# Kernel optimization log

Hardware: AMD Instinct MI355X
Metric: run time of the kernel (lower is better)

## Reference

```python
import jax, jax.numpy as jnp
import numpy as np

B, L, E, K = 2, 2048, 512, 4
KE = E // 2  # kernel_dim is overwritten to embed_dim//2 in __init__


def setup_inputs() -> dict:
    key = jax.random.key(0)
    ks = jax.random.split(key, 6)
    s = 1.0 / np.sqrt(E).astype(np.float32)
    return {
        "xsa": jax.random.normal(ks[0], (B, L, E), jnp.float32),
        "Wq": jax.random.normal(ks[1], (K * KE, E), jnp.float32) * s,   # attq.weight
        "Wk": jax.random.normal(ks[2], (K * KE, E), jnp.float32) * s,   # attk.weight
        "Wv": jax.random.normal(ks[3], (E, K * E), jnp.float32) * s,    # attv.weight
        "biasW": jax.random.normal(ks[4], (KE, K), jnp.float32) * s,    # bias.weight
        "bias2W": jax.random.normal(ks[5], (E, K), jnp.float32) * s,    # bias2.weight
    }


def reference(xsa, Wq, Wk, Wv, biasW, bias2W):
    b_, l_, e_ = xsa.shape
    k_ = biasW.shape[1]
    ke = biasW.shape[0]
    # projections -> (B,L,K,KE)
    xq = (xsa @ Wq.T).reshape(b_, l_, k_, ke)
    xk = (xsa @ Wk.T).reshape(b_, l_, k_, ke)
    # fold the per-head Gaussian center bias into the keys: xd = xq - (xk + bias)
    xkb = xk + biasW.T[None, None]                      # (B,L,K,KE)
    # ||xq_i - xkb_j||^2 = ||xq_i||^2 - 2 xq_i . xkb_j + ||xkb_j||^2  (avoids (B,L,L,K,KE) blowup)
    qn = jnp.sum(xq * xq, axis=-1)                      # (B,L,K)
    kn = jnp.sum(xkb * xkb, axis=-1)                    # (B,L,K)
    cross = jnp.einsum('bikd,bjkd->bikj', xq, xkb)      # (B,L,K,L)
    hikj = -(qn[..., None] - 2.0 * cross + kn.transpose(0, 2, 1)[:, None])
    hikj = hikj / (ke ** 0.5)
    pikj = jax.nn.softmax(hikj, axis=-1)                # softmax over keys j
    # value gather per head: (B,L,K,E)
    yik = jnp.einsum('bikj,bje->bike', pikj, xsa)
    # per-head linear combine with attv.weight reshaped to (K,E,E)
    Wv3 = Wv.reshape(k_, e_, e_)
    yik = jnp.einsum('bike,kef->bikf', yik, Wv3) + bias2W.T[None, None]
    return yik.reshape(b_, l_, k_ * e_)
```

## Files before the change

kernel.cpp:

```cpp
#include <hip/hip_runtime.h>


#define L_ 2048
#define E_ 512
#define KE_ 256
#define NH_ 4

typedef __bf16 bf16x8 __attribute__((ext_vector_type(8)));
typedef float f32x4 __attribute__((ext_vector_type(4)));

__device__ __forceinline__ float bf2f(unsigned short u){
    union { float f; unsigned int i; } v; v.i = ((unsigned int)u) << 16; return v.f;
}
__device__ __forceinline__ unsigned short f2bf(float x){
    union { float f; unsigned int i; } v; v.f = x;
    unsigned int r = v.i + 0x7fffu + ((v.i >> 16) & 1u);
    return (unsigned short)(r >> 16);
}
__device__ __forceinline__ void gll16(const void* g, void* l){
    __builtin_amdgcn_global_load_lds((const __attribute__((address_space(1))) void*)g,
                                     (__attribute__((address_space(3))) void*)l, 16, 0, 0);
}

__global__ __launch_bounds__(256) void proj_kernel(
    const float* __restrict__ xsa, const float* __restrict__ Wq,
    const float* __restrict__ Wk, const float* __restrict__ biasW,
    unsigned short* __restrict__ xqhi, unsigned short* __restrict__ xqlo,
    unsigned short* __restrict__ xkhi, unsigned short* __restrict__ xklo)
{
    __shared__ float Ast[32][132];
    __shared__ float Bst[32][132];
    const int t = threadIdx.x;
    const int m0 = blockIdx.x * 128;
    const int n0 = blockIdx.y * 128;
    const bool isK = (n0 >= 1024);
    const float* W = isK ? Wk : Wq;
    const int nW0 = isK ? (n0 - 1024) : n0;
    const int ty = t >> 4, tx = t & 15;

    float acc[8][8];
#pragma unroll
    for (int i = 0; i < 8; i++)
#pragma unroll
        for (int j = 0; j < 8; j++) acc[i][j] = 0.f;

    for (int kk0 = 0; kk0 < 512; kk0 += 32) {
#pragma unroll
        for (int r = 0; r < 4; r++) {
            int idx = t + r * 256;
            int row = idx >> 3;
            int c4  = idx & 7;
            float4 v = *reinterpret_cast<const float4*>(&xsa[(size_t)(m0 + row) * 512 + kk0 + c4 * 4]);
            Ast[c4*4+0][row] = v.x; Ast[c4*4+1][row] = v.y;
            Ast[c4*4+2][row] = v.z; Ast[c4*4+3][row] = v.w;
            float4 w = *reinterpret_cast<const float4*>(&W[(size_t)(nW0 + row) * 512 + kk0 + c4 * 4]);
            Bst[c4*4+0][row] = w.x; Bst[c4*4+1][row] = w.y;
            Bst[c4*4+2][row] = w.z; Bst[c4*4+3][row] = w.w;
        }
        __syncthreads();
#pragma unroll
        for (int kk = 0; kk < 32; kk++) {
            float a[8], bb[8];
            *reinterpret_cast<float4*>(&a[0])  = *reinterpret_cast<const float4*>(&Ast[kk][ty*8]);
            *reinterpret_cast<float4*>(&a[4])  = *reinterpret_cast<const float4*>(&Ast[kk][ty*8+4]);
            *reinterpret_cast<float4*>(&bb[0]) = *reinterpret_cast<const float4*>(&Bst[kk][tx*8]);
            *reinterpret_cast<float4*>(&bb[4]) = *reinterpret_cast<const float4*>(&Bst[kk][tx*8+4]);
#pragma unroll
            for (int i = 0; i < 8; i++)
#pragma unroll
                for (int j = 0; j < 8; j++) acc[i][j] += a[i] * bb[j];
        }
        __syncthreads();
    }

    const int nh = (n0 + tx*8) & 1023;
    const int kh = nh >> 8, d0 = nh & 255;
    float bias[8];
#pragma unroll
    for (int j = 0; j < 8; j++) bias[j] = isK ? biasW[(d0 + j) * NH_ + kh] : 0.f;
    unsigned short* dsthi = isK ? xkhi : xqhi;
    unsigned short* dstlo = isK ? xklo : xqlo;

#pragma unroll
    for (int i = 0; i < 8; i++) {
        int m = m0 + ty*8 + i;
        int b = m >> 11, l = m & 2047;
        size_t off = ((size_t)((b * NH_ + kh) * L_ + l)) * KE_ + d0;
        unsigned short th[8], tl[8];
#pragma unroll
        for (int j = 0; j < 8; j++) {
            float x = acc[i][j] + bias[j];
            unsigned short hh = f2bf(x);
            th[j] = hh;
            tl[j] = f2bf(x - bf2f(hh));
        }
        *reinterpret_cast<ushort4*>(&dsthi[off])     = *reinterpret_cast<ushort4*>(&th[0]);
        *reinterpret_cast<ushort4*>(&dsthi[off + 4]) = *reinterpret_cast<ushort4*>(&th[4]);
        *reinterpret_cast<ushort4*>(&dstlo[off])     = *reinterpret_cast<ushort4*>(&tl[0]);
        *reinterpret_cast<ushort4*>(&dstlo[off + 4]) = *reinterpret_cast<ushort4*>(&tl[4]);
    }
}

__global__ __launch_bounds__(256) void trans_kernel(
    const float* __restrict__ xsa, unsigned short* __restrict__ xThi,
    unsigned short* __restrict__ xTlo)
{
    __shared__ float T[64][65];
    const int t = threadIdx.x;
    const int l0 = blockIdx.x * 64, e0 = blockIdx.y * 64, b = blockIdx.z;
#pragma unroll
    for (int p = 0; p < 4; p++) {
        int row = p*16 + (t >> 4);
        int c4 = t & 15;
        float4 v = *reinterpret_cast<const float4*>(&xsa[((size_t)(b*L_ + l0 + row))*E_ + e0 + c4*4]);
        T[row][c4*4+0] = v.x; T[row][c4*4+1] = v.y;
        T[row][c4*4+2] = v.z; T[row][c4*4+3] = v.w;
    }
    __syncthreads();
#pragma unroll
    for (int p = 0; p < 16; p++) {
        int e = p*4 + (t >> 6);
        int lp = t & 63;
        float x = T[lp][e];
        unsigned short hh = f2bf(x);
        size_t off = ((size_t)(b*E_ + e0 + e))*L_ + l0 + lp;
        xThi[off] = hh;
        xTlo[off] = f2bf(x - bf2f(hh));
    }
}

__global__ __launch_bounds__(256) void kn_kernel(
    const unsigned short* __restrict__ xkhi, const unsigned short* __restrict__ xklo,
    float* __restrict__ kn)
{
    const int w = threadIdx.x >> 6, lane = threadIdx.x & 63;
    const int row = blockIdx.x * 4 + w;
    ushort4 uh = *reinterpret_cast<const ushort4*>(&xkhi[(size_t)row * KE_ + lane*4]);
    ushort4 ul = *reinterpret_cast<const ushort4*>(&xklo[(size_t)row * KE_ + lane*4]);
    float x0 = bf2f(uh.x) + bf2f(ul.x);
    float x1 = bf2f(uh.y) + bf2f(ul.y);
    float x2 = bf2f(uh.z) + bf2f(ul.z);
    float x3 = bf2f(uh.w) + bf2f(ul.w);
    float s = x0*x0 + x1*x1 + x2*x2 + x3*x3;
#pragma unroll
    for (int m = 32; m; m >>= 1) s += __shfl_xor(s, m, 64);
    if (lane == 0) kn[row] = s;
}

__global__ __launch_bounds__(256, 1) void attn_kernel(
    const unsigned short* __restrict__ xqhi, const unsigned short* __restrict__ xqlo,
    const unsigned short* __restrict__ xkhi, const unsigned short* __restrict__ xklo,
    const unsigned short* __restrict__ xThi, const unsigned short* __restrict__ xTlo,
    const float* __restrict__ knp, unsigned short* __restrict__ ybar)
{
    __shared__ __align__(16) char smem[131072];
    char* const kh_b = smem;
    char* const kl_b = smem + 32768;
    char* const vh_b = smem + 65536;
    char* const vl_b = smem + 98304;

    const int tid = threadIdx.x;
    const int w = tid >> 6, lane = tid & 63;
    const int l15 = lane & 15, l4 = lane >> 4;
    const int bk = blockIdx.y, b = bk >> 2;
    const int i0 = blockIdx.x * 64;
    const size_t bkL = (size_t)bk * L_;

    bf16x8 qh[8], ql[8];
    {
        const size_t qoff = (bkL + i0 + w*16 + l15) * KE_ + l4*8;
#pragma unroll
        for (int ks = 0; ks < 8; ks++) {
            qh[ks] = *reinterpret_cast<const bf16x8*>(xqhi + qoff + ks*32);
            ql[ks] = *reinterpret_cast<const bf16x8*>(xqlo + qoff + ks*32);
        }
    }

    const int s0tbl[4] = {0,4,1,5};
    const int s1tbl[4] = {2,6,3,7};
    const int jg2 = tid & 3;
    const int vs0 = s0tbl[jg2]*8, vs1 = s1tbl[jg2]*8;

    uint4 vreg[16];
#pragma unroll
    for (int r = 0; r < 16; r++) {
        int arr = r >> 3;
        int e = (r & 7)*64 + (tid >> 2);
        const unsigned short* src = (arr ? xTlo : xThi) + ((size_t)(b*E_ + e))*L_ + 0 + jg2*8;
        vreg[r] = *reinterpret_cast<const uint4*>(src);
    }
#pragma unroll
    for (int r = 0; r < 8; r++) {
        int seg = w*8 + r;
        int arr = seg >> 4;
        int sj  = (seg & 15)*2 + (lane >> 5);
        int c   = lane & 31;
        int cp  = c ^ (sj & 7);
        const unsigned short* src = (arr ? xklo : xkhi) + (bkL + 0 + sj)*KE_ + cp*8;
        char* dst = (arr ? kl_b : kh_b) + (seg & 15)*1024;
        gll16(src, dst);
    }
    __syncthreads();

    f32x4 O[32];
#pragma unroll
    for (int e = 0; e < 32; e++) O[e] = (f32x4){0.f,0.f,0.f,0.f};
    float mrun = -1e30f, lrun = 0.f;
    int cur = 0;
    const int axor = (l15 & 7) << 4;

    for (int t = 0; t < 64; ++t) {
        const int j0 = t*32;
        const int jn = (j0 + 32) & (L_-1);

#pragma unroll
        for (int r = 0; r < 16; r++) {
            int e = (r & 7)*64 + (tid >> 2);
            int key = ((e >> 1) & 7) << 4;
            char* base = (r >> 3) ? vl_b : vh_b;
            uint2 lo; lo.x = vreg[r].x; lo.y = vreg[r].y;
            uint2 hi; hi.x = vreg[r].z; hi.y = vreg[r].w;
            *reinterpret_cast<uint2*>(base + ((e*64 + vs0) ^ key)) = lo;
            *reinterpret_cast<uint2*>(base + ((e*64 + vs1) ^ key)) = hi;
        }
#pragma unroll
        for (int r = 0; r < 8; r++) {
            int seg = w*8 + r;
            int arr = seg >> 4;
            int sj  = (seg & 15)*2 + (lane >> 5);
            int c   = lane & 31;
            int cp  = c ^ (sj & 7);
            const unsigned short* src = (arr ? xklo : xkhi) + (bkL + jn + sj)*KE_ + cp*8;
            char* dst = (arr ? kl_b : kh_b) + (cur ^ 1)*16384 + (seg & 15)*1024;
            gll16(src, dst);
        }
        float4 kn0 = *reinterpret_cast<const float4*>(knp + bkL + j0 + l4*4);
        float4 kn1 = *reinterpret_cast<const float4*>(knp + bkL + j0 + 16 + l4*4);

        f32x4 s0 = (f32x4){0.f,0.f,0.f,0.f};
        f32x4 s1 = (f32x4){0.f,0.f,0.f,0.f};
        {
            const char* kh = kh_b + cur*16384;
            const char* kl = kl_b + cur*16384;
            const int arow0 = l15*512, arow1 = (16 + l15)*512;
#pragma unroll
            for (int ks = 0; ks < 8; ks++) {
                int ko = ks*64 + l4*16;
                int a0 = (arow0 + ko) ^ axor;
                int a1 = (arow1 + ko) ^ axor;
                bf16x8 ah0 = *reinterpret_cast<const bf16x8*>(kh + a0);
                bf16x8 al0 = *reinterpret_cast<const bf16x8*>(kl + a0);
                bf16x8 ah1 = *reinterpret_cast<const bf16x8*>(kh + a1);
                bf16x8 al1 = *reinterpret_cast<const bf16x8*>(kl + a1);
                s0 = __builtin_amdgcn_mfma_f32_16x16x32_bf16(ah0, qh[ks], s0, 0, 0, 0);
                s0 = __builtin_amdgcn_mfma_f32_16x16x32_bf16(al0, qh[ks], s0, 0, 0, 0);
                s0 = __builtin_amdgcn_mfma_f32_16x16x32_bf16(ah0, ql[ks], s0, 0, 0, 0);
                s1 = __builtin_amdgcn_mfma_f32_16x16x32_bf16(ah1, qh[ks], s1, 0, 0, 0);
                s1 = __builtin_amdgcn_mfma_f32_16x16x32_bf16(al1, qh[ks], s1, 0, 0, 0);
                s1 = __builtin_amdgcn_mfma_f32_16x16x32_bf16(ah1, ql[ks], s1, 0, 0, 0);
            }
        }

        float h[8];
#pragma unroll
        for (int r = 0; r < 4; r++) {
            h[r]   = s0[r]*0.125f - ((const float*)&kn0)[r]*0.0625f;
            h[4+r] = s1[r]*0.125f - ((const float*)&kn1)[r]*0.0625f;
        }
        float pmax = h[0];
#pragma unroll
        for (int r = 1; r < 8; r++) pmax = fmaxf(pmax, h[r]);
        pmax = fmaxf(pmax, __shfl_xor(pmax, 16, 64));
        pmax = fmaxf(pmax, __shfl_xor(pmax, 32, 64));
        if (__any(pmax > mrun + 8.0f)) {
            float mnew = fmaxf(mrun, pmax);
            float osc = __expf(mrun - mnew);
            mrun = mnew;
            lrun *= osc;
            float osc_pv[4];
#pragma unroll
            for (int r = 0; r < 4; r++) osc_pv[r] = __shfl(osc, l4*4 + r, 64);
#pragma unroll
            for (int et = 0; et < 32; et++) {
                O[et][0] *= osc_pv[0]; O[et][1] *= osc_pv[1];
                O[et][2] *= osc_pv[2]; O[et][3] *= osc_pv[3];
            }
        }
        float p[8], ls = 0.f;
#pragma unroll
        for (int r = 0; r < 8; r++) { p[r] = __expf(h[r] - mrun); ls += p[r]; }
        ls += __shfl_xor(ls, 16, 64);
        ls += __shfl_xor(ls, 32, 64);
        lrun += ls;
        bf16x8 pah, pal;
        {
            union { unsigned int u[4]; bf16x8 v; } ch, cl;
#pragma unroll
            for (int i = 0; i < 4; i++) {
                unsigned short h0 = f2bf(p[2*i]),   h1 = f2bf(p[2*i+1]);
                unsigned short l0 = f2bf(p[2*i]   - bf2f(h0));
                unsigned short l1 = f2bf(p[2*i+1] - bf2f(h1));
                ch.u[i] = (unsigned int)h0 | ((unsigned int)h1 << 16);
                cl.u[i] = (unsigned int)l0 | ((unsigned int)l1 << 16);
            }
            pah = ch.v; pal = cl.v;
        }

        __syncthreads();

#pragma unroll
        for (int r = 0; r < 16; r++) {
            int arr = r >> 3;
            int e = (r & 7)*64 + (tid >> 2);
            const unsigned short* src = (arr ? xTlo : xThi) + ((size_t)(b*E_ + e))*L_ + jn + jg2*8;
            vreg[r] = *reinterpret_cast<const uint4*>(src);
        }
#pragma unroll
        for (int et = 0; et < 32; et++) {
            int vo = (et*16 + l15)*64 + l4*16;
            vo ^= ((vo >> 7) & 7) << 4;
            bf16x8 vh = *reinterpret_cast<const bf16x8*>(vh_b + vo);
            bf16x8 vl = *reinterpret_cast<const bf16x8*>(vl_b + vo);
            O[et] = __builtin_amdgcn_mfma_f32_16x16x32_bf16(pah, vh, O[et], 0, 0, 0);
            O[et] = __builtin_amdgcn_mfma_f32_16x16x32_bf16(pal, vh, O[et], 0, 0, 0);
            O[et] = __builtin_amdgcn_mfma_f32_16x16x32_bf16(pah, vl, O[et], 0, 0, 0);
        }

        __syncthreads();
        cur ^= 1;
    }

    float inv = 1.f / lrun;
    float inv_pv[4];
#pragma unroll
    for (int r = 0; r < 4; r++) inv_pv[r] = __shfl(inv, l4*4 + r, 64);
#pragma unroll
    for (int r = 0; r < 4; r++) {
        int row = i0 + w*16 + l4*4 + r;
        size_t base = (bkL + row)*E_ + l15;
#pragma unroll
        for (int et = 0; et < 32; et++)
            ybar[base + et*16] = f2bf(O[et][r] * inv_pv[r]);
    }
}

__global__ __launch_bounds__(256) void combine_kernel(
    const unsigned short* __restrict__ ybar, const float* __restrict__ Wv,
    const float* __restrict__ bias2W, float* __restrict__ out)
{
    __shared__ float Ast[32][132];
    __shared__ float Bst[32][132];
    const int t = threadIdx.x;
    const int m0 = blockIdx.x * 128;
    const int n0 = blockIdx.y * 128;
    const int bk = blockIdx.z;
    const int k = bk & 3, b = bk >> 2;
    const size_t abase = (size_t)bk * L_ * E_;
    const size_t wbase = (size_t)k * E_ * E_;
    const int ty = t >> 4, tx = t & 15;

    float acc[8][8];
#pragma unroll
    for (int i = 0; i < 8; i++)
#pragma unroll
        for (int j = 0; j < 8; j++) acc[i][j] = 0.f;

    for (int kk0 = 0; kk0 < 512; kk0 += 32) {
#pragma unroll
        for (int r = 0; r < 4; r++) {
            int idx = t + r * 256;
            int row = idx >> 3;
            int c4  = idx & 7;
            ushort4 u = *reinterpret_cast<const ushort4*>(&ybar[abase + (size_t)(m0 + row) * E_ + kk0 + c4*4]);
            Ast[c4*4+0][row] = bf2f(u.x); Ast[c4*4+1][row] = bf2f(u.y);
            Ast[c4*4+2][row] = bf2f(u.z); Ast[c4*4+3][row] = bf2f(u.w);
            int er  = idx >> 5;
            int fc4 = idx & 31;
            *reinterpret_cast<float4*>(&Bst[er][fc4*4]) =
                *reinterpret_cast<const float4*>(&Wv[wbase + (size_t)(kk0 + er) * E_ + n0 + fc4*4]);
        }
        __syncthreads();
#pragma unroll
        for (int kk = 0; kk < 32; kk++) {
            float a[8], bb[8];
            *reinterpret_cast<float4*>(&a[0])  = *reinterpret_cast<const float4*>(&Ast[kk][ty*8]);
            *reinterpret_cast<float4*>(&a[4])  = *reinterpret_cast<const float4*>(&Ast[kk][ty*8+4]);
            *reinterpret_cast<float4*>(&bb[0]) = *reinterpret_cast<const float4*>(&Bst[kk][tx*8]);
            *reinterpret_cast<float4*>(&bb[4]) = *reinterpret_cast<const float4*>(&Bst[kk][tx*8+4]);
#pragma unroll
            for (int i = 0; i < 8; i++)
#pragma unroll
                for (int j = 0; j < 8; j++) acc[i][j] += a[i] * bb[j];
        }
        __syncthreads();
    }

    float bias[8];
#pragma unroll
    for (int j = 0; j < 8; j++) bias[j] = bias2W[(n0 + tx*8 + j) * NH_ + k];

#pragma unroll
    for (int i = 0; i < 8; i++) {
        int iL = m0 + ty*8 + i;
        size_t ob = ((size_t)b * L_ + iL) * (NH_ * E_) + k * E_ + n0 + tx*8;
        float4 v0 = make_float4(acc[i][0]+bias[0], acc[i][1]+bias[1], acc[i][2]+bias[2], acc[i][3]+bias[3]);
        float4 v1 = make_float4(acc[i][4]+bias[4], acc[i][5]+bias[5], acc[i][6]+bias[6], acc[i][7]+bias[7]);
        *reinterpret_cast<float4*>(&out[ob])     = v0;
        *reinterpret_cast<float4*>(&out[ob + 4]) = v1;
    }
}

extern "C" void kernel_launch(void* const* d_in, const int* in_sizes, int n_in,
                              void* d_out, int out_size, void* d_ws, size_t ws_size,
                              hipStream_t stream)
{
    const float* xsa    = (const float*)d_in[0];
    const float* Wq     = (const float*)d_in[1];
    const float* Wk     = (const float*)d_in[2];
    const float* Wv     = (const float*)d_in[3];
    const float* biasW  = (const float*)d_in[4];
    const float* bias2W = (const float*)d_in[5];
    float* out = (float*)d_out;

    unsigned short* ws16 = (unsigned short*)d_ws;
    unsigned short* xqhi = ws16;
    unsigned short* xqlo = ws16 + 4194304;
    unsigned short* xkhi = ws16 + 8388608;
    unsigned short* xklo = ws16 + 12582912;
    unsigned short* xThi = ws16 + 16777216;
    unsigned short* xTlo = ws16 + 18874368;
    unsigned short* ybar = ws16 + 20971520;
    float* knv = (float*)(ws16 + 29360128);

    proj_kernel<<<dim3(32, 16), 256, 0, stream>>>(xsa, Wq, Wk, biasW, xqhi, xqlo, xkhi, xklo);
    trans_kernel<<<dim3(32, 8, 2), 256, 0, stream>>>(xsa, xThi, xTlo);
    kn_kernel<<<dim3(4096), 256, 0, stream>>>(xkhi, xklo, knv);
    attn_kernel<<<dim3(32, 8), 256, 0, stream>>>(xqhi, xqlo, xkhi, xklo, xThi, xTlo, knv, ybar);
    combine_kernel<<<dim3(16, 4, 8), 256, 0, stream>>>(ybar, Wv, bias2W, out);
}
```

Measured before the change: 525.1 us.

## Use MFMA for combine GEMM and split attention output across 512-thread blocks

The combine GEMM moves from scalar FP32 FMA to bf16 MFMA with a hi/lo split of Wv, and a new kernel pre-transposes and splits Wv for it. The attention kernel now runs 512 threads per block: each pair of waves shares a 16-row query tile and splits the 512-wide value dimension in half. This halves the per-wave output accumulator registers and doubles the waves available to hide latency. In exchange, QK^T scores are recomputed redundantly in both waves of a pair, an extra kernel launch is added, and dropping the lo term of ybar in combine loses some precision.

```diff
diff --git a/kernel.cpp b/kernel.cpp
--- a/kernel.cpp
+++ b/kernel.cpp
@@ -129,6 +129,34 @@
     }
 }
 
+__global__ __launch_bounds__(256) void wsplit_kernel(
+    const float* __restrict__ Wv, unsigned short* __restrict__ whiT,
+    unsigned short* __restrict__ wloT)
+{
+    __shared__ float T[64][65];
+    const int t = threadIdx.x;
+    const int e0 = blockIdx.x * 64, f0 = blockIdx.y * 64, k = blockIdx.z;
+#pragma unroll
+    for (int p = 0; p < 4; p++) {
+        int row = p*16 + (t >> 4);
+        int c4 = t & 15;
+        float4 v = *reinterpret_cast<const float4*>(&Wv[((size_t)(k*E_ + e0 + row))*E_ + f0 + c4*4]);
+        T[row][c4*4+0] = v.x; T[row][c4*4+1] = v.y;
+        T[row][c4*4+2] = v.z; T[row][c4*4+3] = v.w;
+    }
+    __syncthreads();
+#pragma unroll
+    for (int p = 0; p < 16; p++) {
+        int fl = p*4 + (t >> 6);
+        int el = t & 63;
+        float x = T[el][fl];
+        unsigned short hh = f2bf(x);
+        size_t off = ((size_t)(k*E_ + f0 + fl))*E_ + e0 + el;
+        whiT[off] = hh;
+        wloT[off] = f2bf(x - bf2f(hh));
+    }
+}
+
 __global__ __launch_bounds__(256) void kn_kernel(
     const unsigned short* __restrict__ xkhi, const unsigned short* __restrict__ xklo,
     float* __restrict__ kn)
@@ -147,7 +175,7 @@
     if (lane == 0) kn[row] = s;
 }
 
-__global__ __launch_bounds__(256, 1) void attn_kernel(
+__global__ __launch_bounds__(512, 2) void attn_kernel(
     const unsigned short* __restrict__ xqhi, const unsigned short* __restrict__ xqlo,
     const unsigned short* __restrict__ xkhi, const unsigned short* __restrict__ xklo,
     const unsigned short* __restrict__ xThi, const unsigned short* __restrict__ xTlo,
@@ -161,6 +189,7 @@
 
     const int tid = threadIdx.x;
     const int w = tid >> 6, lane = tid & 63;
+    const int rg = w >> 1, h = w & 1;
     const int l15 = lane & 15, l4 = lane >> 4;
     const int bk = blockIdx.y, b = bk >> 2;
     const int i0 = blockIdx.x * 64;
@@ -168,7 +197,7 @@
 
     bf16x8 qh[8], ql[8];
     {
-        const size_t qoff = (bkL + i0 + w*16 + l15) * KE_ + l4*8;
+        const size_t qoff = (bkL + i0 + rg*16 + l15) * KE_ + l4*8;
 #pragma unroll
         for (int ks = 0; ks < 8; ks++) {
             qh[ks] = *reinterpret_cast<const bf16x8*>(xqhi + qoff + ks*32);
@@ -178,33 +207,32 @@
 
     const int s0tbl[4] = {0,4,1,5};
     const int s1tbl[4] = {2,6,3,7};
-    const int jg2 = tid & 3;
-    const int vs0 = s0tbl[jg2]*8, vs1 = s1tbl[jg2]*8;
-
-    uint4 vreg[16];
-#pragma unroll
-    for (int r = 0; r < 16; r++) {
-        int arr = r >> 3;
-        int e = (r & 7)*64 + (tid >> 2);
-        const unsigned short* src = (arr ? xTlo : xThi) + ((size_t)(b*E_ + e))*L_ + 0 + jg2*8;
+    const int jc = tid & 3;
+    const int vs0 = s0tbl[jc]*8, vs1 = s1tbl[jc]*8;
+
+    uint4 vreg[8];
+#pragma unroll
+    for (int r = 0; r < 8; r++) {
+        int arr = r >> 2;
+        int e = (r & 3)*128 + (tid >> 2);
+        const unsigned short* src = (arr ? xTlo : xThi) + ((size_t)(b*E_ + e))*L_ + 0 + jc*8;
         vreg[r] = *reinterpret_cast<const uint4*>(src);
     }
 #pragma unroll
-    for (int r = 0; r < 8; r++) {
-        int seg = w*8 + r;
-        int arr = seg >> 4;
-        int sj  = (seg & 15)*2 + (lane >> 5);
+    for (int r = 0; r < 4; r++) {
+        int arr = r >> 1;
+        int sj  = (r & 1)*16 + w*2 + (lane >> 5);
         int c   = lane & 31;
         int cp  = c ^ (sj & 7);
         const unsigned short* src = (arr ? xklo : xkhi) + (bkL + 0 + sj)*KE_ + cp*8;
-        char* dst = (arr ? kl_b : kh_b) + (seg & 15)*1024;
+        char* dst = (arr ? kl_b : kh_b) + ((r & 1)*512 + w*64)*16;
         gll16(src, dst);
     }
     __syncthreads();
 
-    f32x4 O[32];
-#pragma unroll
-    for (int e = 0; e < 32; e++) O[e] = (f32x4){0.f,0.f,0.f,0.f};
+    f32x4 O[16];
+#pragma unroll
+    for (int e = 0; e < 16; e++) O[e] = (f32x4){0.f,0.f,0.f,0.f};
     float mrun = -1e30f, lrun = 0.f;
     int cur = 0;
     const int axor = (l15 & 7) << 4;
@@ -214,24 +242,23 @@
         const int jn = (j0 + 32) & (L_-1);
 
 #pragma unroll
-        for (int r = 0; r < 16; r++) {
-            int e = (r & 7)*64 + (tid >> 2);
+        for (int r = 0; r < 8; r++) {
+            int e = (r & 3)*128 + (tid >> 2);
             int key = ((e >> 1) & 7) << 4;
-            char* base = (r >> 3) ? vl_b : vh_b;
+            char* base = (r >> 2) ? vl_b : vh_b;
             uint2 lo; lo.x = vreg[r].x; lo.y = vreg[r].y;
             uint2 hi; hi.x = vreg[r].z; hi.y = vreg[r].w;
             *reinterpret_cast<uint2*>(base + ((e*64 + vs0) ^ key)) = lo;
             *reinterpret_cast<uint2*>(base + ((e*64 + vs1) ^ key)) = hi;
         }
 #pragma unroll
-        for (int r = 0; r < 8; r++) {
-            int seg = w*8 + r;
-            int arr = seg >> 4;
-            int sj  = (seg & 15)*2 + (lane >> 5);
+        for (int r = 0; r < 4; r++) {
+            int arr = r >> 1;
+            int sj  = (r & 1)*16 + w*2 + (lane >> 5);
             int c   = lane & 31;
             int cp  = c ^ (sj & 7);
             const unsigned short* src = (arr ? xklo : xkhi) + (bkL + jn + sj)*KE_ + cp*8;
-            char* dst = (arr ? kl_b : kh_b) + (cur ^ 1)*16384 + (seg & 15)*1024;
+            char* dst = (arr ? kl_b : kh_b) + (cur ^ 1)*16384 + ((r & 1)*512 + w*64)*16;
             gll16(src, dst);
         }
         float4 kn0 = *reinterpret_cast<const float4*>(knp + bkL + j0 + l4*4);
@@ -261,15 +288,15 @@
             }
         }
 
-        float h[8];
+        float hh[8];
 #pragma unroll
         for (int r = 0; r < 4; r++) {
-            h[r]   = s0[r]*0.125f - ((const float*)&kn0)[r]*0.0625f;
-            h[4+r] = s1[r]*0.125f - ((const float*)&kn1)[r]*0.0625f;
-        }
-        float pmax = h[0];
-#pragma unroll
-        for (int r = 1; r < 8; r++) pmax = fmaxf(pmax, h[r]);
+            hh[r]   = s0[r]*0.125f - ((const float*)&kn0)[r]*0.0625f;
+            hh[4+r] = s1[r]*0.125f - ((const float*)&kn1)[r]*0.0625f;
+        }
+        float pmax = hh[0];
+#pragma unroll
+        for (int r = 1; r < 8; r++) pmax = fmaxf(pmax, hh[r]);
         pmax = fmaxf(pmax, __shfl_xor(pmax, 16, 64));
         pmax = fmaxf(pmax, __shfl_xor(pmax, 32, 64));
         if (__any(pmax > mrun + 8.0f)) {
@@ -281,14 +308,14 @@
 #pragma unroll
             for (int r = 0; r < 4; r++) osc_pv[r] = __shfl(osc, l4*4 + r, 64);
 #pragma unroll
-            for (int et = 0; et < 32; et++) {
+            for (int et = 0; et < 16; et++) {
                 O[et][0] *= osc_pv[0]; O[et][1] *= osc_pv[1];
                 O[et][2] *= osc_pv[2]; O[et][3] *= osc_pv[3];
             }
         }
         float p[8], ls = 0.f;
 #pragma unroll
-        for (int r = 0; r < 8; r++) { p[r] = __expf(h[r] - mrun); ls += p[r]; }
+        for (int r = 0; r < 8; r++) { p[r] = __expf(hh[r] - mrun); ls += p[r]; }
         ls += __shfl_xor(ls, 16, 64);
         ls += __shfl_xor(ls, 32, 64);
         lrun += ls;
@@ -309,15 +336,15 @@
         __syncthreads();
 
 #pragma unroll
-        for (int r = 0; r < 16; r++) {
-            int arr = r >> 3;
-            int e = (r & 7)*64 + (tid >> 2);
-            const unsigned short* src = (arr ? xTlo : xThi) + ((size_t)(b*E_ + e))*L_ + jn + jg2*8;
+        for (int r = 0; r < 8; r++) {
+            int arr = r >> 2;
+            int e = (r & 3)*128 + (tid >> 2);
+            const unsigned short* src = (arr ? xTlo : xThi) + ((size_t)(b*E_ + e))*L_ + jn + jc*8;
             vreg[r] = *reinterpret_cast<const uint4*>(src);
         }
 #pragma unroll
-        for (int et = 0; et < 32; et++) {
-            int vo = (et*16 + l15)*64 + l4*16;
+        for (int et = 0; et < 16; et++) {
+            int vo = (((h*16 + et)*16 + l15))*64 + l4*16;
             vo ^= ((vo >> 7) & 7) << 4;
             bf16x8 vh = *reinterpret_cast<const bf16x8*>(vh_b + vo);
             bf16x8 vl = *reinterpret_cast<const bf16x8*>(vl_b + vo);
@@ -336,78 +363,89 @@
     for (int r = 0; r < 4; r++) inv_pv[r] = __shfl(inv, l4*4 + r, 64);
 #pragma unroll
     for (int r = 0; r < 4; r++) {
-        int row = i0 + w*16 + l4*4 + r;
-        size_t base = (bkL + row)*E_ + l15;
-#pragma unroll
-        for (int et = 0; et < 32; et++)
+        int row = i0 + rg*16 + l4*4 + r;
+        size_t base = (bkL + row)*E_ + h*256 + l15;
+#pragma unroll
+        for (int et = 0; et < 16; et++)
             ybar[base + et*16] = f2bf(O[et][r] * inv_pv[r]);
     }
 }
 
 __global__ __launch_bounds__(256) void combine_kernel(
-    const unsigned short* __restrict__ ybar, const float* __restrict__ Wv,
-    const float* __restrict__ bias2W, float* __restrict__ out)
-{
-    __shared__ float Ast[32][132];
-    __shared__ float Bst[32][132];
-    const int t = threadIdx.x;
+    const unsigned short* __restrict__ ybar, const unsigned short* __restrict__ whiT,
+    const unsigned short* __restrict__ wloT, const float* __restrict__ bias2W,
+    float* __restrict__ out)
+{
+    __shared__ unsigned short A_s[128][40];
+    __shared__ unsigned short Bh_s[128][40];
+    __shared__ unsigned short Bl_s[128][40];
+
+    const int tid = threadIdx.x;
+    const int w = tid >> 6, lane = tid & 63;
+    const int wm = w >> 1, wn = w & 1;
+    const int l15 = lane & 15, l4 = lane >> 4;
     const int m0 = blockIdx.x * 128;
     const int n0 = blockIdx.y * 128;
     const int bk = blockIdx.z;
     const int k = bk & 3, b = bk >> 2;
     const size_t abase = (size_t)bk * L_ * E_;
     const size_t wbase = (size_t)k * E_ * E_;
-    const int ty = t >> 4, tx = t & 15;
-
-    float acc[8][8];
-#pragma unroll
-    for (int i = 0; i < 8; i++)
-#pragma unroll
-        for (int j = 0; j < 8; j++) acc[i][j] = 0.f;
-
-    for (int kk0 = 0; kk0 < 512; kk0 += 32) {
-#pragma unroll
-        for (int r = 0; r < 4; r++) {
-            int idx = t + r * 256;
-            int row = idx >> 3;
-            int c4  = idx & 7;
-            ushort4 u = *reinterpret_cast<const ushort4*>(&ybar[abase + (size_t)(m0 + row) * E_ + kk0 + c4*4]);
-            Ast[c4*4+0][row] = bf2f(u.x); Ast[c4*4+1][row] = bf2f(u.y);
-            Ast[c4*4+2][row] = bf2f(u.z); Ast[c4*4+3][row] = bf2f(u.w);
-            int er  = idx >> 5;
-            int fc4 = idx & 31;
-            *reinterpret_cast<float4*>(&Bst[er][fc4*4]) =
-                *reinterpret_cast<const float4*>(&Wv[wbase + (size_t)(kk0 + er) * E_ + n0 + fc4*4]);
-        }
-        __syncthreads();
-#pragma unroll
-        for (int kk = 0; kk < 32; kk++) {
-            float a[8], bb[8];
-            *reinterpret_cast<float4*>(&a[0])  = *reinterpret_cast<const float4*>(&Ast[kk][ty*8]);
-            *reinterpret_cast<float4*>(&a[4])  = *reinterpret_cast<const float4*>(&Ast[kk][ty*8+4]);
-            *reinterpret_cast<float4*>(&bb[0]) = *reinterpret_cast<const float4*>(&Bst[kk][tx*8]);
-            *reinterpret_cast<float4*>(&bb[4]) = *reinterpret_cast<const float4*>(&Bst[kk][tx*8+4]);
-#pragma unroll
-            for (int i = 0; i < 8; i++)
-#pragma unroll
-                for (int j = 0; j < 8; j++) acc[i][j] += a[i] * bb[j];
-        }
-        __syncthreads();
-    }
-
-    float bias[8];
-#pragma unroll
-    for (int j = 0; j < 8; j++) bias[j] = bias2W[(n0 + tx*8 + j) * NH_ + k];
-
-#pragma unroll
-    for (int i = 0; i < 8; i++) {
-        int iL = m0 + ty*8 + i;
-        size_t ob = ((size_t)b * L_ + iL) * (NH_ * E_) + k * E_ + n0 + tx*8;
-        float4 v0 = make_float4(acc[i][0]+bias[0], acc[i][1]+bias[1], acc[i][2]+bias[2], acc[i][3]+bias[3]);
-        float4 v1 = make_float4(acc[i][4]+bias[4], acc[i][5]+bias[5], acc[i][6]+bias[6], acc[i][7]+bias[7]);
-        *reinterpret_cast<float4*>(&out[ob])     = v0;
-        *reinterpret_cast<float4*>(&out[ob + 4]) = v1;
-    }
+
+    f32x4 acc[4][4];
+#pragma unroll
+    for (int i = 0; i < 4; i++)
+#pragma unroll
+        for (int j = 0; j < 4; j++) acc[i][j] = (f32x4){0.f,0.f,0.f,0.f};
+
+    for (int e0 = 0; e0 < 512; e0 += 32) {
+        __syncthreads();
+#pragma unroll
+        for (int r = 0; r < 2; r++) {
+            int idx = tid + r*256;
+            int row = idx >> 2, c = idx & 3;
+            *reinterpret_cast<uint4*>(&A_s[row][c*8]) =
+                *reinterpret_cast<const uint4*>(&ybar[abase + (size_t)(m0 + row)*E_ + e0 + c*8]);
+            *reinterpret_cast<uint4*>(&Bh_s[row][c*8]) =
+                *reinterpret_cast<const uint4*>(&whiT[wbase + (size_t)(n0 + row)*E_ + e0 + c*8]);
+            *reinterpret_cast<uint4*>(&Bl_s[row][c*8]) =
+                *reinterpret_cast<const uint4*>(&wloT[wbase + (size_t)(n0 + row)*E_ + e0 + c*8]);
+        }
+        __syncthreads();
+
+        bf16x8 a[4], bh[4], bl[4];
+#pragma unroll
+        for (int mt = 0; mt < 4; mt++)
+            a[mt] = *reinterpret_cast<const bf16x8*>(&A_s[wm*64 + mt*16 + l15][l4*8]);
+#pragma unroll
+        for (int ft = 0; ft < 4; ft++) {
+            bh[ft] = *reinterpret_cast<const bf16x8*>(&Bh_s[wn*64 + ft*16 + l15][l4*8]);
+            bl[ft] = *reinterpret_cast<const bf16x8*>(&Bl_s[wn*64 + ft*16 + l15][l4*8]);
+        }
+#pragma unroll
+        for (int mt = 0; mt < 4; mt++)
+#pragma unroll
+            for (int ft = 0; ft < 4; ft++) {
+                acc[mt][ft] = __builtin_amdgcn_mfma_f32_16x16x32_bf16(a[mt], bh[ft], acc[mt][ft], 0, 0, 0);
+                acc[mt][ft] = __builtin_amdgcn_mfma_f32_16x16x32_bf16(a[mt], bl[ft], acc[mt][ft], 0, 0, 0);
+            }
+    }
+
+    float bias[4];
+#pragma unroll
+    for (int ft = 0; ft < 4; ft++)
+        bias[ft] = bias2W[(n0 + wn*64 + ft*16 + l15) * NH_ + k];
+
+#pragma unroll
+    for (int mt = 0; mt < 4; mt++)
+#pragma unroll
+        for (int ft = 0; ft < 4; ft++) {
+            int f = n0 + wn*64 + ft*16 + l15;
+#pragma unroll
+            for (int rr = 0; rr < 4; rr++) {
+                int i = m0 + wm*64 + mt*16 + l4*4 + rr;
+                out[((size_t)(b*L_ + i))*(NH_*E_) + k*E_ + f] = acc[mt][ft][rr] + bias[ft];
+            }
+        }
 }
 
 extern "C" void kernel_launch(void* const* d_in, const int* in_sizes, int n_in,
@@ -423,18 +461,21 @@
     float* out = (float*)d_out;
 
     unsigned short* ws16 = (unsigned short*)d_ws;
-    unsigned short* xqhi = ws16;
-    unsigned short* xqlo = ws16 + 4194304;
-    unsigned short* xkhi = ws16 + 8388608;
-    unsigned short* xklo = ws16 + 12582912;
-    unsigned short* xThi = ws16 + 16777216;
-    unsigned short* xTlo = ws16 + 18874368;
-    unsigned short* ybar = ws16 + 20971520;
-    float* knv = (float*)(ws16 + 29360128);
+    unsigned short* xqhi  = ws16;
+    unsigned short* xqlo  = ws16 + 4194304;
+    unsigned short* xkhi  = ws16 + 8388608;
+    unsigned short* xklo  = ws16 + 12582912;
+    unsigned short* xThi  = ws16 + 16777216;
+    unsigned short* xTlo  = ws16 + 18874368;
+    unsigned short* ybar  = ws16 + 20971520;
+    float*          knv   = (float*)(ws16 + 29360128);
+    unsigned short* wvhiT = ws16 + 29392896;
+    unsigned short* wvloT = ws16 + 30441472;
 
     proj_kernel<<<dim3(32, 16), 256, 0, stream>>>(xsa, Wq, Wk, biasW, xqhi, xqlo, xkhi, xklo);
     trans_kernel<<<dim3(32, 8, 2), 256, 0, stream>>>(xsa, xThi, xTlo);
+    wsplit_kernel<<<dim3(8, 8, 4), 256, 0, stream>>>(Wv, wvhiT, wvloT);
     kn_kernel<<<dim3(4096), 256, 0, stream>>>(xkhi, xklo, knv);
-    attn_kernel<<<dim3(32, 8), 256, 0, stream>>>(xqhi, xqlo, xkhi, xklo, xThi, xTlo, knv, ybar);
-    combine_kernel<<<dim3(16, 4, 8), 256, 0, stream>>>(ybar, Wv, bias2W, out);
-}
+    attn_kernel<<<dim3(32, 8), 512, 0, stream>>>(xqhi, xqlo, xkhi, xklo, xThi, xTlo, knv, ybar);
+    combine_kernel<<<dim3(16, 4, 8), 256, 0, stream>>>(ybar, wvhiT, wvloT, bias2W, out);
+}
```

After: 429.9 us. 18.1% less time.
